# Performance work log

Hardware: AMD Instinct MI355X
Metric: run time of the kernel (lower is better)

Reference implementation:

```python
import jax, jax.numpy as jnp
import numpy as np

IN_FEATURES = 64
OUT_FEATURES = 16
GRID_SIZE = 8
SPLINE_ORDER = 3
GRID_MIN, GRID_MAX = -1.0, 1.0
N = 100000


def make_grid():
    # grid = arange(-spline_order, grid_size+spline_order+1) * m + grid_min, expanded per input feature
    m = (GRID_MAX - GRID_MIN) / GRID_SIZE
    g = jnp.arange(-SPLINE_ORDER, GRID_SIZE + SPLINE_ORDER + 1, dtype=jnp.float32) * m + GRID_MIN
    return jnp.broadcast_to(g, (IN_FEATURES, g.shape[0]))  # [in, gs+2*so+1]


def setup_inputs() -> dict:
    key = jax.random.key(0)
    k1, k2 = jax.random.split(key)
    # x must lie inside the grid range [-1, 1]
    x = jax.random.uniform(k1, (N, IN_FEATURES), dtype=jnp.float32, minval=-1.0, maxval=1.0)
    y = jax.random.normal(k2, (N, IN_FEATURES, OUT_FEATURES), dtype=jnp.float32)
    grid = make_grid()
    return {"x": x, "y": y, "grid": grid}


def bspline_basis(x, grid):
    """Cox-de Boor recursion. x: [N, in], grid: [in, G]. Returns [N, in, gs+so]."""
    xe = x[..., None]  # [N, in, 1]
    # order-0 indicator basis
    b = ((xe >= grid[:, :-1]) & (xe < grid[:, 1:])).astype(x.dtype)  # [N, in, G-1]
    for k in range(1, SPLINE_ORDER + 1):
        left = (xe - grid[:, : -(k + 1)]) / (grid[:, k:-1] - grid[:, : -(k + 1)])
        right = (grid[:, k + 1:] - xe) / (grid[:, k + 1:] - grid[:, 1:-k])
        b = left * b[..., :-1] + right * b[..., 1:]
    return b  # [N, in, gs+so]


def reference(x, y, grid):
    # curve(): least-squares fit of spline-basis coefficients, batched over input features.
    k = bspline_basis(x, grid)            # [N, in, K]
    A = jnp.transpose(k, (1, 0, 2))        # [in, N, K]
    B = jnp.transpose(y, (1, 0, 2))        # [in, N, out]
    # full-rank least squares via normal equations (equivalent to torch.linalg.lstsq solution)
    AtA = jnp.einsum('ink,inl->ikl', A, A)  # [in, K, K]
    AtB = jnp.einsum('ink,ino->iko', A, B)  # [in, K, out]
    X = jnp.linalg.solve(AtA, AtB)          # [in, K, out]
    return jnp.transpose(X, (2, 0, 1))      # [out, in, K]
```

## Files before the change

### kernel.cpp

```cpp
#include <hip/hip_runtime.h>

#define N_ROWS 100000
#define IN_F 64
#define OUT_F 16
#define KB 11
#define SLOTS 216
#define PB (IN_F * SLOTS)
#define RGROUPS 16
#define MAX_NB 1024

__global__ __launch_bounds__(256, 4) void kan_partial(const float* __restrict__ x,
                                                      const float* __restrict__ y,
                                                      float* __restrict__ ws, int nb) {
    __shared__ float kd[IN_F * 12];
    const int tid = threadIdx.x;
    const int f = tid >> 2;
    const int q = tid & 3;
    const int o4 = q * 4;
    float* slot = &kd[f * 12];

    float4 atb[KB];
    float  atA[KB];
#pragma unroll
    for (int kk = 0; kk < KB; ++kk) {
        atb[kk] = make_float4(0.f, 0.f, 0.f, 0.f);
        atA[kk] = 0.f;
    }

    const int per = (N_ROWS + nb - 1) / nb;
    const int lo = blockIdx.x * per;
    const int hi = (lo + per < N_ROWS) ? (lo + per) : N_ROWS;

    if (lo < hi) {
        float xv = 0.f;
        if (q == 0) xv = x[(size_t)lo * IN_F + f];
        float4 y4 = *(const float4*)(y + (size_t)lo * (IN_F * OUT_F) + tid * 4);

        for (int n = lo; n < hi; ++n) {
            const int np = (n + 1 < hi) ? (n + 1) : n;
            float xnext = 0.f;
            if (q == 0) xnext = x[(size_t)np * IN_F + f];
            const float4 ynext = *(const float4*)(y + (size_t)np * (IN_F * OUT_F) + tid * 4);

            if (q == 0) {
                const float tpos = (xv + 1.0f) * 4.0f;
                int c = (int)tpos;
                c = c < 0 ? 0 : (c > 7 ? 7 : c);
                const float u = tpos - (float)c;
                const float omu = 1.0f - u;
                const float b0 = omu * omu * omu * (1.0f / 6.0f);
                const float b3 = u * u * u * (1.0f / 6.0f);
                const float b1 = (0.5f * u - 1.0f) * u * u + (2.0f / 3.0f);
                const float b2 = 1.0f - b0 - b1 - b3;
                const float4 z = make_float4(0.f, 0.f, 0.f, 0.f);
                ((float4*)slot)[0] = z; ((float4*)slot)[1] = z; ((float4*)slot)[2] = z;
                slot[c] = b0; slot[c + 1] = b1; slot[c + 2] = b2; slot[c + 3] = b3;
            }
            const float4 k0 = ((const float4*)slot)[0];
            const float4 k1 = ((const float4*)slot)[1];
            const float4 k2 = ((const float4*)slot)[2];
            const float k[12] = {k0.x, k0.y, k0.z, k0.w, k1.x, k1.y, k1.z, k1.w,
                                 k2.x, k2.y, k2.z, k2.w};

#pragma unroll
            for (int kk = 0; kk < KB; ++kk) {
                atb[kk].x += k[kk] * y4.x;
                atb[kk].y += k[kk] * y4.y;
                atb[kk].z += k[kk] * y4.z;
                atb[kk].w += k[kk] * y4.w;
            }
            if (q == 0) {
#pragma unroll
                for (int a = 0; a < 11; ++a) atA[a] += k[a] * k[a];
            } else if (q == 1) {
#pragma unroll
                for (int a = 0; a < 10; ++a) atA[a] += k[a] * k[a + 1];
            } else if (q == 2) {
#pragma unroll
                for (int a = 0; a < 9; ++a) atA[a] += k[a] * k[a + 2];
            } else {
#pragma unroll
                for (int a = 0; a < 8; ++a) atA[a] += k[a] * k[a + 3];
            }
            xv = xnext;
            y4 = ynext;
        }
    }

    float* base = ws + ((size_t)blockIdx.x * IN_F + f) * SLOTS;
    const int bandBase = (q == 0) ? 0 : (q == 1) ? 11 : (q == 2) ? 21 : 30;
    const int bandCnt = 11 - q;
    for (int m = 0; m < bandCnt; ++m) base[bandBase + m] = atA[m];
#pragma unroll
    for (int kk = 0; kk < KB; ++kk)
        *(float4*)(base + 40 + kk * 16 + o4) = atb[kk];
}

__global__ __launch_bounds__(256) void kan_reduce(float* __restrict__ ws, int nb) {
    const int gid = blockIdx.x * 256 + threadIdx.x;
    const int e = gid % PB;
    const int g = gid / PB;
    float val = 0.f;
#pragma unroll 4
    for (int p = g; p < nb; p += RGROUPS) val += ws[(size_t)p * PB + e];
    ws[((size_t)nb + g) * PB + e] = val;
}

__global__ __launch_bounds__(320) void kan_solve(const float* __restrict__ ws2,
                                                 float* __restrict__ out) {
    __shared__ float M[11][28];
    const int i = blockIdx.x;
    const int tid = threadIdx.x;

    float val = 0.f;
    if (tid < SLOTS) {
#pragma unroll
        for (int g = 0; g < RGROUPS; ++g)
            val += ws2[(size_t)g * PB + (size_t)i * SLOTS + tid];
    }
    {
        const int r = tid / 28, c = tid % 28;
        if (r < 11) M[r][c] = 0.f;
    }
    __syncthreads();
    if (tid < 38) {
        int d, a;
        if (tid < 11)      { d = 0; a = tid; }
        else if (tid < 21) { d = 1; a = tid - 11; }
        else if (tid < 30) { d = 2; a = tid - 21; }
        else               { d = 3; a = tid - 30; }
        M[a][a + d] = val;
        M[a + d][a] = val;
    } else if (tid >= 40 && tid < SLOTS) {
        const int e = tid - 40;
        M[e >> 4][11 + (e & 15)] = val;
    }
    __syncthreads();

    const int rr = tid / 28, cc = tid % 28;
    const bool active = (rr < 11) && (cc < 27);
    for (int p = 0; p < 11; ++p) {
        float pd = 1.f, mpc = 0.f, mrp = 0.f, mrc = 0.f;
        if (active) { pd = M[p][p]; mpc = M[p][cc]; mrp = M[rr][p]; mrc = M[rr][cc]; }
        __syncthreads();
        if (active) {
            const float s = mpc / pd;
            M[rr][cc] = (rr == p) ? s : mrc - mrp * s;
        }
        __syncthreads();
    }

    if (tid < 176) {
        const int o = tid / 11, r2 = tid % 11;
        out[o * (IN_F * KB) + i * KB + r2] = M[r2][11 + o];
    }
}

extern "C" void kernel_launch(void* const* d_in, const int* in_sizes, int n_in,
                              void* d_out, int out_size, void* d_ws, size_t ws_size,
                              hipStream_t stream) {
    const float* x = (const float*)d_in[0];
    const float* y = (const float*)d_in[1];
    float* out = (float*)d_out;
    float* ws  = (float*)d_ws;

    const size_t per_block = (size_t)PB * sizeof(float);
    long cap = (long)(ws_size / per_block) - RGROUPS;
    int nb = (int)(cap < 1 ? 1 : (cap > MAX_NB ? MAX_NB : cap));

    kan_partial<<<nb, 256, 0, stream>>>(x, y, ws, nb);
    kan_reduce<<<(RGROUPS * PB) / 256, 256, 0, stream>>>(ws, nb);
    kan_solve<<<IN_F, 320, 0, stream>>>(ws + (size_t)nb * PB, out);
}
```

Baseline: 579.3 us.

## Fuse partial-sum reduction into solve kernel and deepen row prefetch

Drops the separate reduce kernel. The workspace is relaid out feature-major with padded 256-float slots, so each solve block reduces its own feature's partials using float4 loads and a shared-memory tree. The partial kernel now prefetches two rows ahead instead of one, and spreads the spline basis computation across all four lanes per feature instead of only lane 0. This saves one launch and one pass over the workspace, but each solve block now reduces nb partials serially with only 64 blocks, and prefetching adds register pressure.

```diff
diff --git a/kernel.cpp b/kernel.cpp
--- a/kernel.cpp
+++ b/kernel.cpp
@@ -4,9 +4,7 @@
 #define IN_F 64
 #define OUT_F 16
 #define KB 11
-#define SLOTS 216
-#define PB (IN_F * SLOTS)
-#define RGROUPS 16
+#define SLOTS_P 256
 #define MAX_NB 1024
 
 __global__ __launch_bounds__(256, 4) void kan_partial(const float* __restrict__ x,
@@ -29,33 +27,38 @@
 
     const int per = (N_ROWS + nb - 1) / nb;
     const int lo = blockIdx.x * per;
-    const int hi = (lo + per < N_ROWS) ? (lo + per) : N_ROWS;
+    int hi = lo + per;
+    if (hi > N_ROWS) hi = N_ROWS;
 
     if (lo < hi) {
-        float xv = 0.f;
-        if (q == 0) xv = x[(size_t)lo * IN_F + f];
-        float4 y4 = *(const float4*)(y + (size_t)lo * (IN_F * OUT_F) + tid * 4);
+        const int nrows = hi - lo;
+        const float* xp = x + (size_t)lo * IN_F + f;
+        const float4* yp = (const float4*)(y + (size_t)lo * (IN_F * OUT_F)) + tid;
 
-        for (int n = lo; n < hi; ++n) {
-            const int np = (n + 1 < hi) ? (n + 1) : n;
-            float xnext = 0.f;
-            if (q == 0) xnext = x[(size_t)np * IN_F + f];
-            const float4 ynext = *(const float4*)(y + (size_t)np * (IN_F * OUT_F) + tid * 4);
+        float  x0 = xp[0];
+        float  x1 = (nrows > 1) ? xp[IN_F] : x0;
+        float4 y0 = yp[0];
+        float4 y1 = (nrows > 1) ? yp[256] : y0;
 
-            if (q == 0) {
-                const float tpos = (xv + 1.0f) * 4.0f;
-                int c = (int)tpos;
-                c = c < 0 ? 0 : (c > 7 ? 7 : c);
-                const float u = tpos - (float)c;
-                const float omu = 1.0f - u;
-                const float b0 = omu * omu * omu * (1.0f / 6.0f);
-                const float b3 = u * u * u * (1.0f / 6.0f);
-                const float b1 = (0.5f * u - 1.0f) * u * u + (2.0f / 3.0f);
-                const float b2 = 1.0f - b0 - b1 - b3;
-                const float4 z = make_float4(0.f, 0.f, 0.f, 0.f);
-                ((float4*)slot)[0] = z; ((float4*)slot)[1] = z; ((float4*)slot)[2] = z;
-                slot[c] = b0; slot[c + 1] = b1; slot[c + 2] = b2; slot[c + 3] = b3;
-            }
+        for (int n = 0; n < nrows; ++n) {
+            const int npf = (n + 2 < nrows) ? (n + 2) : (nrows - 1);
+            const float  x2 = xp[(size_t)npf * IN_F];
+            const float4 y2 = yp[(size_t)npf * 256];
+
+            const float tpos = (x0 + 1.0f) * 4.0f;
+            int c = (int)tpos;
+            c = c < 0 ? 0 : (c > 7 ? 7 : c);
+            const float u = tpos - (float)c;
+            const float omu = 1.0f - u;
+            const float b0 = omu * omu * omu * (1.0f / 6.0f);
+            const float b3 = u * u * u * (1.0f / 6.0f);
+            const float b1 = (0.5f * u - 1.0f) * u * u + (2.0f / 3.0f);
+            const float b2 = 1.0f - b0 - b1 - b3;
+
+            if (q < 3) ((float4*)slot)[q] = make_float4(0.f, 0.f, 0.f, 0.f);
+            const float bq = (q == 0) ? b0 : ((q == 1) ? b1 : ((q == 2) ? b2 : b3));
+            slot[c + q] = bq;
+
             const float4 k0 = ((const float4*)slot)[0];
             const float4 k1 = ((const float4*)slot)[1];
             const float4 k2 = ((const float4*)slot)[2];
@@ -64,10 +67,10 @@
 
 #pragma unroll
             for (int kk = 0; kk < KB; ++kk) {
-                atb[kk].x += k[kk] * y4.x;
-                atb[kk].y += k[kk] * y4.y;
-                atb[kk].z += k[kk] * y4.z;
-                atb[kk].w += k[kk] * y4.w;
+                atb[kk].x += k[kk] * y0.x;
+                atb[kk].y += k[kk] * y0.y;
+                atb[kk].z += k[kk] * y0.z;
+                atb[kk].w += k[kk] * y0.w;
             }
             if (q == 0) {
 #pragma unroll
@@ -82,12 +85,13 @@
 #pragma unroll
                 for (int a = 0; a < 8; ++a) atA[a] += k[a] * k[a + 3];
             }
-            xv = xnext;
-            y4 = ynext;
+
+            x0 = x1; x1 = x2;
+            y0 = y1; y1 = y2;
         }
     }
 
-    float* base = ws + ((size_t)blockIdx.x * IN_F + f) * SLOTS;
+    float* base = ws + ((size_t)f * nb + blockIdx.x) * SLOTS_P;
     const int bandBase = (q == 0) ? 0 : (q == 1) ? 11 : (q == 2) ? 21 : 30;
     const int bandCnt = 11 - q;
     for (int m = 0; m < bandCnt; ++m) base[bandBase + m] = atA[m];
@@ -96,31 +100,38 @@
         *(float4*)(base + 40 + kk * 16 + o4) = atb[kk];
 }
 
-__global__ __launch_bounds__(256) void kan_reduce(float* __restrict__ ws, int nb) {
-    const int gid = blockIdx.x * 256 + threadIdx.x;
-    const int e = gid % PB;
-    const int g = gid / PB;
-    float val = 0.f;
-#pragma unroll 4
-    for (int p = g; p < nb; p += RGROUPS) val += ws[(size_t)p * PB + e];
-    ws[((size_t)nb + g) * PB + e] = val;
-}
-
-__global__ __launch_bounds__(320) void kan_solve(const float* __restrict__ ws2,
-                                                 float* __restrict__ out) {
-    __shared__ float M[11][28];
+__global__ __launch_bounds__(320) void kan_solve(const float* __restrict__ ws,
+                                                 float* __restrict__ out, int nb) {
+    __shared__ float4 sred[256];
+    __shared__ float  ssum[SLOTS_P];
+    __shared__ float  M[11][28];
     const int i = blockIdx.x;
     const int tid = threadIdx.x;
 
-    float val = 0.f;
-    if (tid < SLOTS) {
-#pragma unroll
-        for (int g = 0; g < RGROUPS; ++g)
-            val += ws2[(size_t)g * PB + (size_t)i * SLOTS + tid];
+    if (tid < 256) {
+        const float4* slab = (const float4*)(ws + (size_t)i * nb * SLOTS_P);
+        const int s4 = tid & 63;
+        float4 acc = make_float4(0.f, 0.f, 0.f, 0.f);
+        for (int b = tid >> 6; b < nb; b += 4) {
+            const float4 v = slab[(size_t)b * 64 + s4];
+            acc.x += v.x; acc.y += v.y; acc.z += v.z; acc.w += v.w;
+        }
+        sred[tid] = acc;
     }
     {
         const int r = tid / 28, c = tid % 28;
         if (r < 11) M[r][c] = 0.f;
+    }
+    __syncthreads();
+    if (tid < 64) {
+        const float4 a = sred[tid], b = sred[tid + 64],
+                     c = sred[tid + 128], d = sred[tid + 192];
+        float4 s;
+        s.x = (a.x + b.x) + (c.x + d.x);
+        s.y = (a.y + b.y) + (c.y + d.y);
+        s.z = (a.z + b.z) + (c.z + d.z);
+        s.w = (a.w + b.w) + (c.w + d.w);
+        ((float4*)ssum)[tid] = s;
     }
     __syncthreads();
     if (tid < 38) {
@@ -129,11 +140,12 @@
         else if (tid < 21) { d = 1; a = tid - 11; }
         else if (tid < 30) { d = 2; a = tid - 21; }
         else               { d = 3; a = tid - 30; }
-        M[a][a + d] = val;
-        M[a + d][a] = val;
-    } else if (tid >= 40 && tid < SLOTS) {
+        const float v = ssum[tid];
+        M[a][a + d] = v;
+        M[a + d][a] = v;
+    } else if (tid >= 40 && tid < 216) {
         const int e = tid - 40;
-        M[e >> 4][11 + (e & 15)] = val;
+        M[e >> 4][11 + (e & 15)] = ssum[tid];
     }
     __syncthreads();
 
@@ -164,11 +176,10 @@
     float* out = (float*)d_out;
     float* ws  = (float*)d_ws;
 
-    const size_t per_block = (size_t)PB * sizeof(float);
-    long cap = (long)(ws_size / per_block) - RGROUPS;
+    const size_t per_nb = (size_t)IN_F * SLOTS_P * sizeof(float);
+    long cap = (long)(ws_size / per_nb);
     int nb = (int)(cap < 1 ? 1 : (cap > MAX_NB ? MAX_NB : cap));
 
     kan_partial<<<nb, 256, 0, stream>>>(x, y, ws, nb);
-    kan_reduce<<<(RGROUPS * PB) / 256, 256, 0, stream>>>(ws, nb);
-    kan_solve<<<IN_F, 320, 0, stream>>>(ws + (size_t)nb * PB, out);
+    kan_solve<<<IN_F, 320, 0, stream>>>(ws, out, nb);
 }
```

After: 667.1 us. 15.2% more time.
